# Kernel tuning notes

Hardware: AMD Instinct MI355X
Metric: run time of the kernel (lower is better)

## Reference

```python
import jax, jax.numpy as jnp
import numpy as np

B, S, V = 32, 4096, 128
NSEG = S // 2 + 2  # rising-edge boundaries are at most ceil(S/2), so seg_id <= S//2


def sinusoidal_pe(seq_len, d_model, dtype=jnp.float32):
    pos = jnp.arange(seq_len, dtype=jnp.float32)[:, None]              # [S,1]
    div = jnp.exp(jnp.arange(0, d_model, 2, dtype=jnp.float32) * (-np.log(10000.0) / d_model))
    pe = jnp.zeros((seq_len, d_model), dtype=jnp.float32)
    pe = pe.at[:, 0::2].set(jnp.sin(pos * div))
    pe = pe.at[:, 1::2].set(jnp.cos(pos * div))
    return pe.astype(dtype)


def setup_inputs() -> dict:
    key = jax.random.key(0)
    ks = jax.random.split(key, 8)
    return {
        "bert_output": jax.random.normal(ks[0], (B, S, V), dtype=jnp.float32),
        "startpos": jax.random.uniform(ks[1], (B, S), dtype=jnp.float32),
        "Wq": jax.random.normal(ks[2], (V, V), dtype=jnp.float32) * 0.02,
        "bq": jax.random.normal(ks[3], (V,), dtype=jnp.float32) * 0.02,
        "Wk": jax.random.normal(ks[4], (V, V), dtype=jnp.float32) * 0.02,
        "bk": jax.random.normal(ks[5], (V,), dtype=jnp.float32) * 0.02,
        "Wv": jax.random.normal(ks[6], (V, V), dtype=jnp.float32) * 0.02,
        "bv": jax.random.normal(ks[7], (V,), dtype=jnp.float32) * 0.02,
    }


def reference(bert_output, startpos, Wq, bq, Wk, bk, Wv, bv):
    b, s, v = bert_output.shape
    pe = sinusoidal_pe(s, v, bert_output.dtype)
    # positionembedding2 then positionembedding1 (eval mode -> dropout is identity)
    x1 = bert_output + pe          # what gets concatenated at the end
    xseq = x1 + pe                 # per-row sequence fed to pooling and attention (pe added twice, as in source)

    # Rising-edge segment boundaries: mask[t] = start[t]>=0.5 and (t==0 or start[t-1]<0.5)
    ge = startpos >= 0.5
    prev = jnp.concatenate([jnp.zeros((b, 1), dtype=bool), ge[:, :-1]], axis=1)
    mask = ge & (~prev)                                     # [B,S]
    seg_id = jnp.cumsum(mask.astype(jnp.int32), axis=1)     # inclusive cumsum: token's segment index
    num_time_seq = jnp.sum(mask.astype(jnp.int32), axis=1) + 1

    # Mean-pool xseq per segment (segment_sum over flattened (batch, seg) ids)
    flat_ids = (jnp.arange(b, dtype=jnp.int32)[:, None] * NSEG + seg_id).reshape(-1)
    seg_sum = jax.ops.segment_sum(xseq.reshape(b * s, v), flat_ids, num_segments=b * NSEG)
    seg_cnt = jax.ops.segment_sum(jnp.ones((b * s,), xseq.dtype), flat_ids, num_segments=b * NSEG)
    seg_mean = (seg_sum / jnp.maximum(seg_cnt, 1.0)[:, None]).reshape(b, NSEG, v)

    # AttentionLayer (no softmax): out = (q @ K^T / sqrt(S)) @ V  ==  q @ (K^T V) / sqrt(S)
    q_seg = seg_mean @ Wq.T + bq                             # [B,NSEG,V]
    k = xseq @ Wk.T + bk                                     # [B,S,V]
    vv = xseq @ Wv.T + bv                                    # [B,S,V]
    kv = jnp.einsum("bsv,bsw->bvw", k, vv)                  # [B,V,V]
    q_tok = jnp.take_along_axis(q_seg, seg_id[..., None], axis=1)  # broadcast segment q to tokens [B,S,V]
    attn = jnp.einsum("btv,bvw->btw", q_tok, kv) / np.sqrt(float(s)).astype(np.float32)

    out = jnp.concatenate([attn, x1], axis=-1)               # [B,S,2V]
    return out, num_time_seq
```

## Files before the change

kernel.cpp:

```cpp
#include <hip/hip_runtime.h>
#include <hip/hip_bf16.h>

#define BB 32
#define SS 4096
#define VV 128
#define NSEG 2050
#define OUT_TAIL (BB*SS*2*VV)

#define PE_F      0u
#define SEGID_F   524288u
#define NSEGS_F   655360u
#define WQTA_F    655392u
#define WKA_F     671904u
#define ZT_F      688416u
#define ZB_F      966944u
#define GPART_F   2036000u
#define SSUM_F    6234400u
#define SCNT_F    14631200u
#define SGLB_F    14696800u
#define SEGSTART_F 14700896u
#define ZT_BYTE     ((size_t)ZT_F*4)
#define LDS_MAIN    132624

using bfrag8 = __attribute__((ext_vector_type(8))) short;
using usvec8 = __attribute__((ext_vector_type(8))) unsigned short;
using f32x4  = __attribute__((ext_vector_type(4))) float;

__device__ __forceinline__ unsigned short f2bf(float v){
  unsigned int u = __float_as_uint(v);
  u += 0x7fffu + ((u >> 16) & 1u);
  return (unsigned short)(u >> 16);
}
__device__ __forceinline__ unsigned short f2bf_hw(float v){
  return __bfloat16_as_ushort(__float2bfloat16(v));
}
__device__ __forceinline__ float bf2f(unsigned short h){
  return __uint_as_float(((unsigned int)h) << 16);
}

__global__ __launch_bounds__(1024) void k_init(const float* __restrict__ Wq, const float* __restrict__ bq,
                                               const float* __restrict__ Wk, const float* __restrict__ bk,
                                               const float* __restrict__ sp,
                                               float* __restrict__ ws, float* __restrict__ out){
  int bx = blockIdx.x, tid = threadIdx.x;
  if (bx < 32){
    int b = bx;
    __shared__ int wtot[16];
    const float* row = sp + (size_t)b*SS;
    float4 v4 = *(const float4*)(row + tid*4);
    float pv = (tid == 0) ? 0.f : row[tid*4 - 1];
    bool g0 = v4.x >= 0.5f, g1 = v4.y >= 0.5f, g2 = v4.z >= 0.5f, g3 = v4.w >= 0.5f;
    bool gp = (tid == 0) ? false : (pv >= 0.5f);
    int m0 = (g0 && !gp) ? 1 : 0;
    int m1 = (g1 && !g0) ? 1 : 0;
    int m2 = (g2 && !g1) ? 1 : 0;
    int m3 = (g3 && !g2) ? 1 : 0;
    int c0 = m0, c1 = c0+m1, c2 = c1+m2, c3 = c2+m3;
    int lane = tid & 63, wave = tid >> 6;
    int v = c3;
    #pragma unroll
    for (int off = 1; off < 64; off <<= 1){
      int u = __shfl_up(v, off);
      if (lane >= off) v += u;
    }
    if (lane == 63) wtot[wave] = v;
    __syncthreads();
    if (tid < 16){
      int x = wtot[tid];
      #pragma unroll
      for (int off = 1; off < 16; off <<= 1){
        int u = __shfl_up(x, off);
        if (tid >= off) x += u;
      }
      wtot[tid] = x;
    }
    __syncthreads();
    int woff = (wave == 0) ? 0 : wtot[wave-1];
    int excl = woff + v - c3;
    int4 o; o.x = excl+c0; o.y = excl+c1; o.z = excl+c2; o.w = excl+c3;
    *(int4*)((int*)ws + SEGID_F + (size_t)b*SS + tid*4) = o;
    int* sst = (int*)ws + SEGSTART_F + (size_t)b*(NSEG+1);
    if (m0) sst[o.x] = tid*4 + 0;
    if (m1) sst[o.y] = tid*4 + 1;
    if (m2) sst[o.z] = tid*4 + 2;
    if (m3) sst[o.w] = tid*4 + 3;
    if (tid == 0) sst[0] = 0;
    int total = wtot[15];
    for (int g = total + 1 + tid; g <= NSEG; g += 1024) sst[g] = SS;
    if (tid == 1023){
      ((int*)ws)[NSEGS_F + b] = total + 1;
      out[OUT_TAIL + b] = (float)(total + 1);
    }
    return;
  }
  if (bx < 288){
    int gid = (bx - 32)*1024 + tid;
    int t = gid >> 6, i = gid & 63;
    float dv = __expf(-0.14391156831212787f * (float)i);
    float ang = (float)t * dv;
    float s, c;
    __sincosf(ang, &s, &c);
    float2 o; o.x = s; o.y = c;
    ((float2*)(ws + PE_F))[(size_t)t*64 + i] = o;
  } else {
    int gid = (bx - 288)*1024 + tid;
    if (gid < 16384){
      int vv = gid >> 7, a = gid & 127;
      ws[WQTA_F + vv*128 + a] = Wq[a*128 + vv];
    } else if (gid < 16512){
      int a = gid - 16384;
      ws[WQTA_F + 128*128 + a] = bq[a];
    } else if (gid < 32896){
      int e = gid - 16512; int a = e >> 7, i = e & 127;
      ws[WKA_F + a*129 + i] = Wk[a*128 + i];
    } else if (gid < 33024){
      int a = gid - 32896;
      ws[WKA_F + a*129 + 128] = bk[a];
    }
  }
}

__global__ __launch_bounds__(1024) void k_main(const float* __restrict__ bert,
                                               float* __restrict__ ws,
                                               float* __restrict__ out){
  extern __shared__ char smem[];
  float* segacc = (float*)(smem + 65536);
  float* cntacc = (float*)(smem + 65536 + 66048);
  unsigned short* lseg = (unsigned short*)(smem + 65536 + 66048 + 516);

  const int tid = threadIdx.x;
  const int b = blockIdx.y, chunk = blockIdx.x;
  const int fgrp4 = tid & 31, trow = tid >> 5;

  const int* segid = (const int*)ws + SEGID_F + (size_t)b*SS;
  const float* pe = ws + PE_F;

  const int wave = tid >> 6, lane = tid & 63;
  const int mi = wave >> 1, njb = (wave & 1) * 4;
  const int l15 = lane & 15, l4 = lane >> 4;
  f32x4 acc[4];
  #pragma unroll
  for (int q = 0; q < 4; ++q) acc[q] = (f32x4){0.f,0.f,0.f,0.f};
  float sp_part = 0.f;
  const int sf = tid & 127, sgrp = tid >> 7;

  for (int sub = 0; sub < 2; ++sub){
    const int t0 = chunk*512 + sub*256;
    int seg0 = segid[t0];
    if (tid < 256) lseg[tid] = (unsigned short)(segid[t0 + tid] - seg0);
    int nl = segid[t0 + 255] - seg0 + 1;
    for (int idx = tid; idx < nl*32; idx += 1024) ((f32x4*)segacc)[idx] = (f32x4){0.f,0.f,0.f,0.f};
    if (tid < nl) cntacc[tid] = 0.f;
    __syncthreads();

    const int tb = t0 + trow*8;
    const float* bp = bert + ((size_t)(b*SS) + tb)*VV + fgrp4*4;
    const float* pp = pe + (size_t)tb*VV + fgrp4*4;
    float* op = out + ((size_t)(b*SS) + tb)*(2*VV) + VV + fgrp4*4;

    f32x4 racc = (f32x4){0.f,0.f,0.f,0.f};
    unsigned short xb[8][4];
    int cur = lseg[trow*8];
    float runlen = 0.f;
    #pragma unroll
    for (int i = 0; i < 8; ++i){
      int ls = lseg[trow*8 + i];
      if (ls != cur){
        #pragma unroll
        for (int j = 0; j < 4; ++j) unsafeAtomicAdd(&segacc[cur*128 + fgrp4*4 + j], racc[j]);
        if (fgrp4 == 0) unsafeAtomicAdd(&cntacc[cur], runlen);
        racc = (f32x4){0.f,0.f,0.f,0.f}; runlen = 0.f; cur = ls;
      }
      f32x4 bv = __builtin_nontemporal_load((const f32x4*)(bp + i*VV));
      f32x4 pv = *(const f32x4*)(pp + i*VV);
      f32x4 x1 = bv + pv;
      __builtin_nontemporal_store(x1, (f32x4*)(op + i*2*VV));
      f32x4 x = x1 + pv;
      racc += x;
      #pragma unroll
      for (int j = 0; j < 4; ++j) xb[i][j] = f2bf_hw(x[j]);
      runlen += 1.f;
    }
    #pragma unroll
    for (int j = 0; j < 4; ++j) unsafeAtomicAdd(&segacc[cur*128 + fgrp4*4 + j], racc[j]);
    if (fgrp4 == 0) unsafeAtomicAdd(&cntacc[cur], runlen);

    #pragma unroll
    for (int j = 0; j < 4; ++j){
      int f = fgrp4*4 + j;
      int sw = (f ^ (f >> 2)) & 7;
      usvec8 v;
      #pragma unroll
      for (int i = 0; i < 8; ++i) v[i] = xb[i][j];
      *(usvec8*)(smem + f*512 + ((trow ^ sw) << 4)) = v;
    }
    __syncthreads();

    float* srow = ws + SSUM_F + ((size_t)(b*NSEG) + seg0)*128;
    for (int idx = tid; idx < nl*32; idx += 1024){
      int r = idx >> 5, c4 = idx & 31;
      f32x4 v = ((f32x4*)segacc)[idx];
      if (r == 0 || r == nl-1){
        #pragma unroll
        for (int j = 0; j < 4; ++j) unsafeAtomicAdd(&srow[r*128 + c4*4 + j], v[j]);
      } else {
        *(f32x4*)(srow + r*128 + c4*4) = v;
      }
    }
    if (tid < nl){
      float c = cntacc[tid];
      float* cp = ws + SCNT_F + (size_t)b*NSEG + seg0 + tid;
      if (tid == 0 || tid == nl-1) unsafeAtomicAdd(cp, c);
      else *cp = c;
    }
    for (int r = sgrp; r < nl; r += 8) sp_part += segacc[r*128 + sf];

    #pragma unroll
    for (int kk = 0; kk < 8; ++kk){
      int gr = kk*4 + l4;
      int fa = mi*16 + l15;
      bfrag8 aF = *(const bfrag8*)(smem + fa*512 + ((gr ^ ((fa ^ (fa>>2)) & 7)) << 4));
      #pragma unroll
      for (int q = 0; q < 4; ++q){
        int fb = (njb + q)*16 + l15;
        bfrag8 bF = *(const bfrag8*)(smem + fb*512 + ((gr ^ ((fb ^ (fb>>2)) & 7)) << 4));
        acc[q] = __builtin_amdgcn_mfma_f32_16x16x32_bf16(aF, bF, acc[q], 0, 0, 0);
      }
    }
    __syncthreads();
  }

  segacc[tid] = sp_part;
  __syncthreads();
  if (tid < 128){
    float s = 0.f;
    #pragma unroll
    for (int k = 0; k < 8; ++k) s += segacc[tid + 128*k];
    unsafeAtomicAdd(ws + SGLB_F + b*128 + tid, s);
  }

  float* gp = ws + GPART_F + ((size_t)(b*8 + chunk) << 14);
  #pragma unroll
  for (int q = 0; q < 4; ++q){
    #pragma unroll
    for (int r = 0; r < 4; ++r){
      int row = mi*16 + l4*4 + r;
      int col = (njb + q)*16 + l15;
      gp[row*128 + col] = acc[q][r];
    }
  }
}

__global__ __launch_bounds__(256) void k_fused(float* __restrict__ ws,
                                               const float* __restrict__ Wv,
                                               const float* __restrict__ bv){
  __shared__ unsigned short Al[64*136];
  __shared__ unsigned short Bl[129*136];
  __shared__ float svals[128];
  __shared__ float bvv[64];
  int b = blockIdx.x, r0 = blockIdx.y*64, tid = threadIdx.x;
  const float* sg = ws + SGLB_F + (size_t)b*128;
  int wave = tid >> 6, lane = tid & 63, l15 = lane & 15, l4 = lane >> 4;

  {
    const f32x4* gq = (const f32x4*)(ws + GPART_F + ((size_t)(b*8) << 14));
    for (int e = tid; e < 4096; e += 256){
      f32x4 a = (f32x4){0.f,0.f,0.f,0.f};
      #pragma unroll
      for (int c = 0; c < 8; ++c) a += gq[((size_t)c << 12) + e];
      int row = e >> 5, c4 = e & 31;
      unsigned short* dst = &Bl[row*136 + c4*4];
      dst[0]=f2bf(a[0]); dst[1]=f2bf(a[1]); dst[2]=f2bf(a[2]); dst[3]=f2bf(a[3]);
    }
    if (tid < 128) Bl[128*136 + tid] = f2bf(sg[tid]);
  }
  {
    int m = tid >> 2;
    int ks = (tid & 3) * 34;
    int ke = min(128, ks + 34);
    for (int k = ks; k < ke; ++k) Al[m*136 + k] = f2bf(Wv[(size_t)(r0+m)*128 + k]);
  }
  if (tid < 128) svals[tid] = sg[tid];
  if (tid >= 128 && tid < 192) bvv[tid-128] = bv[r0 + tid - 128];
  __syncthreads();

  f32x4 acc[9];

  #pragma unroll
  for (int j = 0; j < 9; ++j) acc[j] = (f32x4){0.f,0.f,0.f,0.f};
  #pragma unroll
  for (int kk = 0; kk < 4; ++kk){
    int k = kk*32 + l4*8;
    bfrag8 aF = *(const bfrag8*)&Al[(wave*16 + l15)*136 + k];
    #pragma unroll
    for (int j = 0; j < 9; ++j){
      bfrag8 bF = *(const bfrag8*)&Bl[(j*16 + l15)*136 + k];
      acc[j] = __builtin_amdgcn_mfma_f32_16x16x32_bf16(aF, bF, acc[j], 0, 0, 0);
    }
  }
  #pragma unroll
  for (int j = 0; j < 9; ++j){
    #pragma unroll
    for (int r = 0; r < 4; ++r){
      int lrow = wave*16 + l4*4 + r;
      int n = j*16 + l15;
      if (n < 129){
        float sx = (n < 128) ? svals[n] : 4096.0f;
        Al[lrow*136 + n] = f2bf(acc[j][r] + bvv[lrow]*sx);
      }
    }
  }
  __syncthreads();

  for (int n = tid >> 1; n < 128; n += 128){
    int ks = (tid & 1) * 65;
    int ke = min(129, ks + 65);
    const float* src = ws + WKA_F + (size_t)n*129;
    for (int k = ks; k < ke; ++k) Bl[n*136 + k] = f2bf(src[k]);
  }
  __syncthreads();

  #pragma unroll
  for (int j = 0; j < 9; ++j) acc[j] = (f32x4){0.f,0.f,0.f,0.f};
  #pragma unroll
  for (int kk = 0; kk < 4; ++kk){
    int k = kk*32 + l4*8;
    bfrag8 aF = *(const bfrag8*)&Al[(wave*16 + l15)*136 + k];
    #pragma unroll
    for (int j = 0; j < 8; ++j){
      bfrag8 bF = *(const bfrag8*)&Bl[(j*16 + l15)*136 + k];
      acc[j] = __builtin_amdgcn_mfma_f32_16x16x32_bf16(aF, bF, acc[j], 0, 0, 0);
    }
  }
  #pragma unroll
  for (int j = 0; j < 8; ++j){
    #pragma unroll
    for (int r = 0; r < 4; ++r){
      int lrow = wave*16 + l4*4 + r;
      int n = j*16 + l15;
      float v = acc[j][r] + bf2f(Al[lrow*136 + 128]) * bf2f(Bl[n*136 + 128]);
      acc[j][r] = v;
    }
  }
  #pragma unroll
  for (int j = 0; j < 8; ++j){
    #pragma unroll
    for (int r = 0; r < 4; ++r){
      int lrow = wave*16 + l4*4 + r;
      int n = j*16 + l15;
      if (n < 128) Al[lrow*136 + n] = f2bf(acc[j][r]);
    }
  }
  __syncthreads();

  for (int n = tid >> 1; n < 129; n += 128){
    int ks = (tid & 1) * 65;
    int ke = min(128, ks + 65);
    const float* src = ws + WQTA_F + (size_t)n*128;
    for (int k = ks; k < ke; ++k) Bl[n*136 + k] = f2bf(src[k]);
  }
  __syncthreads();

  #pragma unroll
  for (int j = 0; j < 9; ++j) acc[j] = (f32x4){0.f,0.f,0.f,0.f};
  #pragma unroll
  for (int kk = 0; kk < 4; ++kk){
    int k = kk*32 + l4*8;
    bfrag8 aF = *(const bfrag8*)&Al[(wave*16 + l15)*136 + k];
    #pragma unroll
    for (int j = 0; j < 9; ++j){
      bfrag8 bF = *(const bfrag8*)&Bl[(j*16 + l15)*136 + k];
      acc[j] = __builtin_amdgcn_mfma_f32_16x16x32_bf16(aF, bF, acc[j], 0, 0, 0);
    }
  }
  unsigned short* zt = (unsigned short*)((char*)ws + ZT_BYTE);
  #pragma unroll
  for (int j = 0; j < 9; ++j){
    #pragma unroll
    for (int r = 0; r < 4; ++r){
      int lrow = wave*16 + l4*4 + r;
      int m = r0 + lrow;
      int n = j*16 + l15;
      float z = acc[j][r] * 0.015625f;
      if (n < 128) zt[(size_t)b*17408 + m*136 + n] = f2bf(z);
      else if (n == 128) ws[ZB_F + (size_t)b*128 + m] = z;
    }
  }
}

__global__ __launch_bounds__(256) void k_attn(float* __restrict__ ws, float* __restrict__ out){
  int b = blockIdx.y, g0 = blockIdx.x * 64, tid = threadIdx.x;
  int nseg = ((const int*)ws)[NSEGS_F + b];
  if (g0 >= nseg) return;
  __shared__ unsigned short Albs[64*136];
  __shared__ __align__(16) char bufB[128*136*2];
  unsigned short* Blbs = (unsigned short*)bufB;
  float* attl = (float*)bufB;
  __shared__ float zbs[128];
  __shared__ int sstart[65];
  if (tid < 65){
    int g = g0 + tid;
    sstart[tid] = (g <= NSEG) ? ((const int*)ws)[SEGSTART_F + (size_t)b*(NSEG+1) + g] : SS;
  }
  {
    int row = tid >> 2, part = tid & 3;
    int g = g0 + row;
    float rc = 1.f;
    const float* ssum = ws + SSUM_F + ((size_t)(b*NSEG + g))*128;
    if (g < NSEG){ float c = ws[SCNT_F + (size_t)b*NSEG + g]; rc = 1.f / fmaxf(c, 1.f); }
    #pragma unroll
    for (int j = 0; j < 8; ++j){
      int cix = part*32 + j*4;
      float4 v;
      if (g < NSEG) v = *(const float4*)(ssum + cix);
      else { v.x=0.f; v.y=0.f; v.z=0.f; v.w=0.f; }
      unsigned short* dst = &Albs[row*136 + cix];
      dst[0] = f2bf(v.x*rc); dst[1] = f2bf(v.y*rc); dst[2] = f2bf(v.z*rc); dst[3] = f2bf(v.w*rc);
    }
  }
  {
    const unsigned int* src = (const unsigned int*)((const char*)ws + ZT_BYTE + (size_t)b*34816);
    unsigned int* dst = (unsigned int*)Blbs;
    for (int i = tid; i < 8704; i += 256) dst[i] = src[i];
  }
  if (tid < 128) zbs[tid] = ws[ZB_F + (size_t)b*128 + tid];
  __syncthreads();
  int wave = tid >> 6, lane = tid & 63, l15 = lane & 15, l4 = lane >> 4;
  f32x4 acc[8];
  #pragma unroll
  for (int q = 0; q < 8; ++q) acc[q] = (f32x4){0.f,0.f,0.f,0.f};
  #pragma unroll
  for (int kk = 0; kk < 4; ++kk){
    int k = kk*32 + l4*8;
    bfrag8 aF = *(const bfrag8*)&Albs[(wave*16 + l15)*136 + k];
    #pragma unroll
    for (int q = 0; q < 8; ++q){
      bfrag8 bF = *(const bfrag8*)&Blbs[(q*16 + l15)*136 + k];
      acc[q] = __builtin_amdgcn_mfma_f32_16x16x32_bf16(aF, bF, acc[q], 0, 0, 0);
    }
  }
  __syncthreads();
  #pragma unroll
  for (int q = 0; q < 8; ++q){
    int w = q*16 + l15;
    float zb = zbs[w];
    #pragma unroll
    for (int r = 0; r < 4; ++r){
      int row = wave*16 + l4*4 + r;
      attl[row*128 + w] = acc[q][r] + zb;
    }
  }
  __syncthreads();
  int lane5 = tid & 31, grp = tid >> 5;
  float* ob4 = out + (size_t)b*SS*(2*VV) + lane5*4;
  for (int gg = 0; gg < 64; ++gg){
    int ts = sstart[gg], te = sstart[gg+1];
    if (ts >= te) continue;
    f32x4 v4 = *(const f32x4*)&attl[gg*128 + lane5*4];
    for (int t = ts + grp; t < te; t += 8){
      __builtin_nontemporal_store(v4, (f32x4*)(ob4 + (size_t)t*(2*VV)));
    }
  }
}

extern "C" void kernel_launch(void* const* d_in, const int* in_sizes, int n_in,
                              void* d_out, int out_size, void* d_ws, size_t ws_size,
                              hipStream_t stream) {
  const float* bert     = (const float*)d_in[0];
  const float* startpos = (const float*)d_in[1];
  const float* Wq       = (const float*)d_in[2];
  const float* bq       = (const float*)d_in[3];
  const float* Wk       = (const float*)d_in[4];
  const float* bk       = (const float*)d_in[5];
  const float* Wv       = (const float*)d_in[6];
  const float* bv       = (const float*)d_in[7];
  float* out = (float*)d_out;
  float* ws  = (float*)d_ws;

  (void)hipFuncSetAttribute(reinterpret_cast<const void*>(k_main),
                            hipFuncAttributeMaxDynamicSharedMemorySize, LDS_MAIN);

  k_init<<<321, 1024, 0, stream>>>(Wq, bq, Wk, bk, startpos, ws, out);
  k_main<<<dim3(8, 32), 1024, LDS_MAIN, stream>>>(bert, ws, out);
  k_fused<<<dim3(32, 2), 256, 0, stream>>>(ws, Wv, bv);
  k_attn<<<dim3(33, 32), 256, 0, stream>>>(ws, out);
}
```

Before: 264.8 us.

## Fold init kernel into main: recompute segment ids and PE inline

Removes the separate init kernel. Each main block now recomputes the per-batch rising-edge scan into LDS, computes the sinusoidal positional encoding on the fly with sincos instead of loading a precomputed table, and the fused kernel reads the Wk/Wq weights directly, transposing Wq on the fly. This saves a kernel launch plus the global round-trips for segment ids, the PE table and the weight copies. In exchange, every one of the 8 chunk blocks per batch repeats the scan, each element adds transcendental work, and the strided Wq reads are uncoalesced.

Result: no change. 269.2 us (+1.7%).

```diff
diff --git a/kernel.cpp b/kernel.cpp
--- a/kernel.cpp
+++ b/kernel.cpp
@@ -7,11 +7,7 @@
 #define NSEG 2050
 #define OUT_TAIL (BB*SS*2*VV)
 
-#define PE_F      0u
-#define SEGID_F   524288u
 #define NSEGS_F   655360u
-#define WQTA_F    655392u
-#define WKA_F     671904u
 #define ZT_F      688416u
 #define ZB_F      966944u
 #define GPART_F   2036000u
@@ -20,7 +16,7 @@
 #define SGLB_F    14696800u
 #define SEGSTART_F 14700896u
 #define ZT_BYTE     ((size_t)ZT_F*4)
-#define LDS_MAIN    132624
+#define LDS_MAIN    140816
 
 using bfrag8 = __attribute__((ext_vector_type(8))) short;
 using usvec8 = __attribute__((ext_vector_type(8))) unsigned short;
@@ -38,14 +34,23 @@
   return __uint_as_float(((unsigned int)h) << 16);
 }
 
-__global__ __launch_bounds__(1024) void k_init(const float* __restrict__ Wq, const float* __restrict__ bq,
-                                               const float* __restrict__ Wk, const float* __restrict__ bk,
+__global__ __launch_bounds__(1024) void k_main(const float* __restrict__ bert,
                                                const float* __restrict__ sp,
-                                               float* __restrict__ ws, float* __restrict__ out){
-  int bx = blockIdx.x, tid = threadIdx.x;
-  if (bx < 32){
-    int b = bx;
-    __shared__ int wtot[16];
+                                               float* __restrict__ ws,
+                                               float* __restrict__ out){
+  extern __shared__ char smem[];
+  float* segacc = (float*)(smem + 65536);
+  float* cntacc = (float*)(smem + 65536 + 66048);
+  unsigned short* lseg = (unsigned short*)(smem + 132100);
+  unsigned short* segid_lds = (unsigned short*)(smem + 132624);
+  __shared__ int wtot[16];
+
+  const int tid = threadIdx.x;
+  const int b = blockIdx.y, chunk = blockIdx.x;
+  const int fgrp4 = tid & 31, trow = tid >> 5;
+  const int wave = tid >> 6, lane = tid & 63;
+
+  {
     const float* row = sp + (size_t)b*SS;
     float4 v4 = *(const float4*)(row + tid*4);
     float pv = (tid == 0) ? 0.f : row[tid*4 - 1];
@@ -56,7 +61,6 @@
     int m2 = (g2 && !g1) ? 1 : 0;
     int m3 = (g3 && !g2) ? 1 : 0;
     int c0 = m0, c1 = c0+m1, c2 = c1+m2, c3 = c2+m3;
-    int lane = tid & 63, wave = tid >> 6;
     int v = c3;
     #pragma unroll
     for (int off = 1; off < 64; off <<= 1){
@@ -77,65 +81,30 @@
     __syncthreads();
     int woff = (wave == 0) ? 0 : wtot[wave-1];
     int excl = woff + v - c3;
-    int4 o; o.x = excl+c0; o.y = excl+c1; o.z = excl+c2; o.w = excl+c3;
-    *(int4*)((int*)ws + SEGID_F + (size_t)b*SS + tid*4) = o;
-    int* sst = (int*)ws + SEGSTART_F + (size_t)b*(NSEG+1);
-    if (m0) sst[o.x] = tid*4 + 0;
-    if (m1) sst[o.y] = tid*4 + 1;
-    if (m2) sst[o.z] = tid*4 + 2;
-    if (m3) sst[o.w] = tid*4 + 3;
-    if (tid == 0) sst[0] = 0;
-    int total = wtot[15];
-    for (int g = total + 1 + tid; g <= NSEG; g += 1024) sst[g] = SS;
-    if (tid == 1023){
-      ((int*)ws)[NSEGS_F + b] = total + 1;
-      out[OUT_TAIL + b] = (float)(total + 1);
-    }
-    return;
-  }
-  if (bx < 288){
-    int gid = (bx - 32)*1024 + tid;
-    int t = gid >> 6, i = gid & 63;
-    float dv = __expf(-0.14391156831212787f * (float)i);
-    float ang = (float)t * dv;
-    float s, c;
-    __sincosf(ang, &s, &c);
-    float2 o; o.x = s; o.y = c;
-    ((float2*)(ws + PE_F))[(size_t)t*64 + i] = o;
-  } else {
-    int gid = (bx - 288)*1024 + tid;
-    if (gid < 16384){
-      int vv = gid >> 7, a = gid & 127;
-      ws[WQTA_F + vv*128 + a] = Wq[a*128 + vv];
-    } else if (gid < 16512){
-      int a = gid - 16384;
-      ws[WQTA_F + 128*128 + a] = bq[a];
-    } else if (gid < 32896){
-      int e = gid - 16512; int a = e >> 7, i = e & 127;
-      ws[WKA_F + a*129 + i] = Wk[a*128 + i];
-    } else if (gid < 33024){
-      int a = gid - 32896;
-      ws[WKA_F + a*129 + 128] = bk[a];
-    }
-  }
-}
-
-__global__ __launch_bounds__(1024) void k_main(const float* __restrict__ bert,
-                                               float* __restrict__ ws,
-                                               float* __restrict__ out){
-  extern __shared__ char smem[];
-  float* segacc = (float*)(smem + 65536);
-  float* cntacc = (float*)(smem + 65536 + 66048);
-  unsigned short* lseg = (unsigned short*)(smem + 65536 + 66048 + 516);
-
-  const int tid = threadIdx.x;
-  const int b = blockIdx.y, chunk = blockIdx.x;
-  const int fgrp4 = tid & 31, trow = tid >> 5;
-
-  const int* segid = (const int*)ws + SEGID_F + (size_t)b*SS;
-  const float* pe = ws + PE_F;
-
-  const int wave = tid >> 6, lane = tid & 63;
+    segid_lds[tid*4+0] = (unsigned short)(excl+c0);
+    segid_lds[tid*4+1] = (unsigned short)(excl+c1);
+    segid_lds[tid*4+2] = (unsigned short)(excl+c2);
+    segid_lds[tid*4+3] = (unsigned short)(excl+c3);
+    if (chunk == 7){
+      int* sst = (int*)ws + SEGSTART_F + (size_t)b*(NSEG+1);
+      if (m0) sst[excl+c0] = tid*4 + 0;
+      if (m1) sst[excl+c1] = tid*4 + 1;
+      if (m2) sst[excl+c2] = tid*4 + 2;
+      if (m3) sst[excl+c3] = tid*4 + 3;
+      if (tid == 0) sst[0] = 0;
+      int total = wtot[15];
+      for (int g = total + 1 + tid; g <= NSEG; g += 1024) sst[g] = SS;
+      if (tid == 1023){
+        ((int*)ws)[NSEGS_F + b] = total + 1;
+        out[OUT_TAIL + b] = (float)(total + 1);
+      }
+    }
+    __syncthreads();
+  }
+
+  const float dv0 = __expf(-0.14391156831212787f * (float)(fgrp4*2));
+  const float dv1 = __expf(-0.14391156831212787f * (float)(fgrp4*2 + 1));
+
   const int mi = wave >> 1, njb = (wave & 1) * 4;
   const int l15 = lane & 15, l4 = lane >> 4;
   f32x4 acc[4];
@@ -146,16 +115,15 @@
 
   for (int sub = 0; sub < 2; ++sub){
     const int t0 = chunk*512 + sub*256;
-    int seg0 = segid[t0];
-    if (tid < 256) lseg[tid] = (unsigned short)(segid[t0 + tid] - seg0);
-    int nl = segid[t0 + 255] - seg0 + 1;
+    int seg0 = segid_lds[t0];
+    if (tid < 256) lseg[tid] = (unsigned short)(segid_lds[t0 + tid] - seg0);
+    int nl = (int)segid_lds[t0 + 255] - seg0 + 1;
     for (int idx = tid; idx < nl*32; idx += 1024) ((f32x4*)segacc)[idx] = (f32x4){0.f,0.f,0.f,0.f};
     if (tid < nl) cntacc[tid] = 0.f;
     __syncthreads();
 
     const int tb = t0 + trow*8;
     const float* bp = bert + ((size_t)(b*SS) + tb)*VV + fgrp4*4;
-    const float* pp = pe + (size_t)tb*VV + fgrp4*4;
     float* op = out + ((size_t)(b*SS) + tb)*(2*VV) + VV + fgrp4*4;
 
     f32x4 racc = (f32x4){0.f,0.f,0.f,0.f};
@@ -172,7 +140,11 @@
         racc = (f32x4){0.f,0.f,0.f,0.f}; runlen = 0.f; cur = ls;
       }
       f32x4 bv = __builtin_nontemporal_load((const f32x4*)(bp + i*VV));
-      f32x4 pv = *(const f32x4*)(pp + i*VV);
+      float tf = (float)(tb + i);
+      float s0, cq0, s1, cq1;
+      __sincosf(tf*dv0, &s0, &cq0);
+      __sincosf(tf*dv1, &s1, &cq1);
+      f32x4 pv = (f32x4){s0, cq0, s1, cq1};
       f32x4 x1 = bv + pv;
       __builtin_nontemporal_store(x1, (f32x4*)(op + i*2*VV));
       f32x4 x = x1 + pv;
@@ -253,7 +225,11 @@
 
 __global__ __launch_bounds__(256) void k_fused(float* __restrict__ ws,
                                                const float* __restrict__ Wv,
-                                               const float* __restrict__ bv){
+                                               const float* __restrict__ bv,
+                                               const float* __restrict__ Wk,
+                                               const float* __restrict__ bk,
+                                               const float* __restrict__ Wq,
+                                               const float* __restrict__ bq){
   __shared__ unsigned short Al[64*136];
   __shared__ unsigned short Bl[129*136];
   __shared__ float svals[128];
@@ -315,8 +291,8 @@
   for (int n = tid >> 1; n < 128; n += 128){
     int ks = (tid & 1) * 65;
     int ke = min(129, ks + 65);
-    const float* src = ws + WKA_F + (size_t)n*129;
-    for (int k = ks; k < ke; ++k) Bl[n*136 + k] = f2bf(src[k]);
+    for (int k = ks; k < ke; ++k)
+      Bl[n*136 + k] = f2bf(k < 128 ? Wk[(size_t)n*128 + k] : bk[n]);
   }
   __syncthreads();
 
@@ -356,8 +332,8 @@
   for (int n = tid >> 1; n < 129; n += 128){
     int ks = (tid & 1) * 65;
     int ke = min(128, ks + 65);
-    const float* src = ws + WQTA_F + (size_t)n*128;
-    for (int k = ks; k < ke; ++k) Bl[n*136 + k] = f2bf(src[k]);
+    for (int k = ks; k < ke; ++k)
+      Bl[n*136 + k] = f2bf(n < 128 ? Wq[(size_t)k*128 + n] : bq[k]);
   }
   __syncthreads();
 
@@ -480,8 +456,7 @@
   (void)hipFuncSetAttribute(reinterpret_cast<const void*>(k_main),
                             hipFuncAttributeMaxDynamicSharedMemorySize, LDS_MAIN);
 
-  k_init<<<321, 1024, 0, stream>>>(Wq, bq, Wk, bk, startpos, ws, out);
-  k_main<<<dim3(8, 32), 1024, LDS_MAIN, stream>>>(bert, ws, out);
-  k_fused<<<dim3(32, 2), 256, 0, stream>>>(ws, Wv, bv);
+  k_main<<<dim3(8, 32), 1024, LDS_MAIN, stream>>>(bert, startpos, ws, out);
+  k_fused<<<dim3(32, 2), 256, 0, stream>>>(ws, Wv, bv, Wk, bk, Wq, bq);
   k_attn<<<dim3(33, 32), 256, 0, stream>>>(ws, out);
 }
```
